# Optimization experiments

Hardware: AMD Instinct MI355X
Metric: run time of the kernel (lower is better)

## Reference

```python
import jax, jax.numpy as jnp
import numpy as np


def _ln(x, g, b, eps=1e-5):
    mu = jnp.mean(x, axis=-1, keepdims=True)
    var = jnp.mean((x - mu) ** 2, axis=-1, keepdims=True)
    return (x - mu) / jnp.sqrt(var + eps) * g + b


def _cell(x, h, c, Wih, Whh, bih, bhh):
    # torch LSTM gate order: i, f, g, o
    gates = x @ Wih.T + h @ Whh.T + bih + bhh
    i, f, g, o = jnp.split(gates, 4, axis=-1)
    c_new = jax.nn.sigmoid(f) * c + jax.nn.sigmoid(i) * jnp.tanh(g)
    h_new = jax.nn.sigmoid(o) * jnp.tanh(c_new)
    return h_new, c_new


def _forward(physical, target_seq, enc_W1, enc_b1, enc_ln1_g, enc_ln1_b, enc_W2, enc_b2,
             enc_ln2_g, enc_ln2_b, Wih0, Whh0, bih0, bhh0, Wih1, Whh1, bih1, bhh1,
             ln_g, ln_b, proj_W, proj_b, head_W1, head_b1, head_W2, head_b2, init_input):
    B, T = target_seq.shape
    Hd = proj_b.shape[0]
    # physical encoder -> initial hidden (dropout in eval mode)
    e = jax.nn.relu(_ln(physical @ enc_W1.T + enc_b1, enc_ln1_g, enc_ln1_b))
    h0 = jnp.tanh(_ln(e @ enc_W2.T + enc_b2, enc_ln2_g, enc_ln2_b))  # (B,H)
    h_init = jnp.broadcast_to(h0, (2, 2, B, Hd))  # (layer, direction, B, H)
    c_init = jnp.zeros((2, 2, B, Hd), dtype=h0.dtype)
    # teacher forcing ratio = 1.0 -> inputs are known ahead of time
    x0 = jnp.broadcast_to(init_input, (B, 1))
    xs = jnp.concatenate([x0[None], jnp.swapaxes(target_seq, 0, 1)[:-1, :, None]], axis=0)  # (T,B,1)

    def step(carry, inp):
        h, c, prev = carry
        x, t = inp
        h0f, c0f = _cell(x, h[0, 0], c[0, 0], Wih0[0], Whh0[0], bih0[0], bhh0[0])
        h0b, c0b = _cell(x, h[0, 1], c[0, 1], Wih0[1], Whh0[1], bih0[1], bhh0[1])
        o0 = jnp.concatenate([h0f, h0b], axis=-1)  # (B,2H)
        h1f, c1f = _cell(o0, h[1, 0], c[1, 0], Wih1[0], Whh1[0], bih1[0], bhh1[0])
        h1b, c1b = _cell(o0, h[1, 1], c[1, 1], Wih1[1], Whh1[1], bih1[1], bhh1[1])
        out = _ln(jnp.concatenate([h1f, h1b], axis=-1), ln_g, ln_b)  # (B,2H)
        proj = out @ proj_W.T + proj_b  # (B,H)
        pred = jax.nn.relu(proj @ head_W1.T + head_b1) @ head_W2.T + head_b2  # (B,1)
        pred = jnp.where(t > 0, 0.8 * pred + 0.2 * prev, pred)
        h_new = jnp.stack([jnp.stack([h0f, h0b]), jnp.stack([h1f, h1b])])
        c_new = jnp.stack([jnp.stack([c0f, c0b]), jnp.stack([c1f, c1b])])
        return (h_new, c_new, pred), pred[:, 0]

    _, preds = jax.lax.scan(step, (h_init, c_init, jnp.zeros((B, 1), h0.dtype)),
                            (xs, jnp.arange(T)))
    return jnp.swapaxes(preds, 0, 1)  # (B,T)


def setup_inputs():
    B, P, Hd, T = 512, 16, 128, 128
    ks = iter(jax.random.split(jax.random.key(0), 40))
    rn = lambda shape, s=0.05: jax.random.normal(next(ks), shape, dtype=jnp.float32) * s
    return {
        "physical": jax.random.normal(next(ks), (B, P), dtype=jnp.float32),
        "target_seq": jax.random.normal(next(ks), (B, T), dtype=jnp.float32),
        "enc_W1": rn((2 * Hd, P)), "enc_b1": jnp.zeros((2 * Hd,), jnp.float32),
        "enc_ln1_g": jnp.ones((2 * Hd,), jnp.float32), "enc_ln1_b": jnp.zeros((2 * Hd,), jnp.float32),
        "enc_W2": rn((Hd, 2 * Hd)), "enc_b2": jnp.zeros((Hd,), jnp.float32),
        "enc_ln2_g": jnp.ones((Hd,), jnp.float32), "enc_ln2_b": jnp.zeros((Hd,), jnp.float32),
        "Wih0": rn((2, 4 * Hd, 1)), "Whh0": rn((2, 4 * Hd, Hd)),
        "bih0": jnp.zeros((2, 4 * Hd), jnp.float32), "bhh0": jnp.zeros((2, 4 * Hd), jnp.float32),
        "Wih1": rn((2, 4 * Hd, 2 * Hd)), "Whh1": rn((2, 4 * Hd, Hd)),
        "bih1": jnp.zeros((2, 4 * Hd), jnp.float32), "bhh1": jnp.zeros((2, 4 * Hd), jnp.float32),
        "ln_g": jnp.ones((2 * Hd,), jnp.float32), "ln_b": jnp.zeros((2 * Hd,), jnp.float32),
        "proj_W": rn((Hd, 2 * Hd)), "proj_b": jnp.zeros((Hd,), jnp.float32),
        "head_W1": rn((Hd, Hd)), "head_b1": jnp.zeros((Hd,), jnp.float32),
        "head_W2": rn((1, Hd)), "head_b2": jnp.zeros((1,), jnp.float32),
        "init_input": rn((1,), 0.02),
    }


def reference(physical, target_seq, enc_W1, enc_b1, enc_ln1_g, enc_ln1_b, enc_W2, enc_b2,
              enc_ln2_g, enc_ln2_b, Wih0, Whh0, bih0, bhh0, Wih1, Whh1, bih1, bhh1,
              ln_g, ln_b, proj_W, proj_b, head_W1, head_b1, head_W2, head_b2, init_input):
    return _forward(physical, target_seq, enc_W1, enc_b1, enc_ln1_g, enc_ln1_b, enc_W2, enc_b2,
                    enc_ln2_g, enc_ln2_b, Wih0, Whh0, bih0, bhh0, Wih1, Whh1, bih1, bhh1,
                    ln_g, ln_b, proj_W, proj_b, head_W1, head_b1, head_W2, head_b2, init_input)
```

## Files before the change

### kernel.cpp

```cpp
#include <hip/hip_runtime.h>
#include <hip/hip_bf16.h>

#define BB 512
#define TT 128

typedef unsigned short u16;
typedef short v8s __attribute__((ext_vector_type(8)));
typedef float f32x4 __attribute__((ext_vector_type(4)));

__device__ __forceinline__ u16 f2bf(float x){
  union { float f; unsigned int u; } v; v.f = x;
  unsigned int r = (v.u + 0x7fffu + ((v.u >> 16) & 1u)) >> 16;
  return (u16)r;
}
__device__ __forceinline__ float bf2f(u16 u){
  union { unsigned int i; float f; } v; v.i = ((unsigned int)u) << 16; return v.f;
}
__device__ __forceinline__ uint2 pack4(f32x4 a){
  uint2 r;
  r.x = (unsigned)f2bf(a[0]) | ((unsigned)f2bf(a[1]) << 16);
  r.y = (unsigned)f2bf(a[2]) | ((unsigned)f2bf(a[3]) << 16);
  return r;
}
__device__ __forceinline__ float rcp_f(float x){ return __builtin_amdgcn_rcpf(x); }
__device__ __forceinline__ float sigm(float x){
  return rcp_f(1.f + __expf(-x));
}
__device__ __forceinline__ float tanh_f(float x){
  float e = __expf(-2.f * fabsf(x));
  float r = (1.f - e) * rcp_f(1.f + e);
  return copysignf(r, x);
}
__device__ __forceinline__ void bar_lds(){
  __builtin_amdgcn_sched_barrier(0);
  asm volatile("s_waitcnt lgkmcnt(0)" ::: "memory");
  __builtin_amdgcn_s_barrier();
  __builtin_amdgcn_sched_barrier(0);
}

__global__ __launch_bounds__(256) void k_prep(
    const float* tseq, const float* init_in,
    const float* Wih0, const float* Whh0, const float* bih0, const float* bhh0,
    const float* Wih1, const float* Whh1, const float* bih1, const float* bhh1,
    const float* projW, const float* hW1,
    float* xs, u16* W0p, u16* W1ip, u16* W1hp, u16* projWp, u16* hW1p,
    float* bias0, float* bias1, float* wv0)
{
  int tid = blockIdx.x * blockDim.x + threadIdx.x;
  int stride = gridDim.x * blockDim.x;
  for (int i = tid; i < TT*BB; i += stride){
    int t = i / BB, b = i % BB;
    xs[i] = (t == 0) ? init_in[0] : tseq[b*TT + (t-1)];
  }
  for (int i = tid; i < 2*512*128; i += stride){
    int d = i / (512*128), r = i % (512*128);
    int j = r / 128, k = r % 128;
    int dst = ((((d*32 + (j>>4))*4 + (k>>5))*64) + ((j&15) + 16*((k&31)>>3)))*8 + (k&7);
    W0p[dst]  = f2bf(Whh0[i]);
    W1hp[dst] = f2bf(Whh1[i]);
  }
  for (int i = tid; i < 2*512*256; i += stride){
    int d = i / (512*256), r = i % (512*256);
    int j = r / 256, k = r % 256;
    int dst = ((((d*32 + (j>>4))*8 + (k>>5))*64) + ((j&15) + 16*((k&31)>>3)))*8 + (k&7);
    W1ip[dst] = f2bf(Wih1[i]);
  }
  for (int i = tid; i < 128*256; i += stride){
    int j = i / 256, k = i % 256;
    int dst = ((((j>>4)*8 + (k>>5))*64) + ((j&15) + 16*((k&31)>>3)))*8 + (k&7);
    projWp[dst] = f2bf(projW[i]);
  }
  for (int i = tid; i < 128*128; i += stride){
    int j = i / 128, k = i % 128;
    int dst = ((((j>>4)*4 + (k>>5))*64) + ((j&15) + 16*((k&31)>>3)))*8 + (k&7);
    hW1p[dst] = f2bf(hW1[i]);
  }
  for (int i = tid; i < 2*512; i += stride){
    bias0[i] = bih0[i] + bhh0[i];
    bias1[i] = bih1[i] + bhh1[i];
    wv0[i]   = Wih0[i];
  }
}

__global__ __launch_bounds__(256) void k_enc(
    const float* phys, const float* W1, const float* b1, const float* g1, const float* be1,
    const float* W2, const float* b2, const float* g2, const float* be2, float* h0enc)
{
  __shared__ float eL[8][256];
  int tid = threadIdx.x;
  int rr = tid >> 5, sub = tid & 31;
  int r = blockIdx.x * 8 + rr;
  float x[16];
#pragma unroll
  for (int k = 0; k < 16; ++k) x[k] = phys[r*16 + k];
  float y[8];
#pragma unroll
  for (int jj = 0; jj < 8; ++jj){
    int j = sub*8 + jj;
    float s = b1[j];
#pragma unroll
    for (int k = 0; k < 16; ++k) s += x[k] * W1[j*16 + k];
    y[jj] = s;
  }
  float sum = 0.f, sq = 0.f;
#pragma unroll
  for (int jj = 0; jj < 8; ++jj){ sum += y[jj]; sq += y[jj]*y[jj]; }
#pragma unroll
  for (int m = 16; m >= 1; m >>= 1){ sum += __shfl_xor(sum, m, 32); sq += __shfl_xor(sq, m, 32); }
  float mu = sum / 256.f;
  float rs = rsqrtf(sq / 256.f - mu*mu + 1e-5f);
#pragma unroll
  for (int jj = 0; jj < 8; ++jj){
    int j = sub*8 + jj;
    eL[rr][j] = fmaxf((y[jj] - mu) * rs * g1[j] + be1[j], 0.f);
  }
  __syncthreads();
  float y2[4];
#pragma unroll
  for (int jj = 0; jj < 4; ++jj){
    int j2 = sub*4 + jj;
    float s = b2[j2];
    const float* wrow = W2 + j2*256;
    for (int k = 0; k < 256; k += 4)
      s += eL[rr][k]*wrow[k] + eL[rr][k+1]*wrow[k+1] + eL[rr][k+2]*wrow[k+2] + eL[rr][k+3]*wrow[k+3];
    y2[jj] = s;
  }
  sum = 0.f; sq = 0.f;
#pragma unroll
  for (int jj = 0; jj < 4; ++jj){ sum += y2[jj]; sq += y2[jj]*y2[jj]; }
#pragma unroll
  for (int m = 16; m >= 1; m >>= 1){ sum += __shfl_xor(sum, m, 32); sq += __shfl_xor(sq, m, 32); }
  mu = sum / 128.f;
  rs = rsqrtf(sq / 128.f - mu*mu + 1e-5f);
#pragma unroll
  for (int jj = 0; jj < 4; ++jj){
    int j2 = sub*4 + jj;
    h0enc[r*128 + j2] = tanh_f((y2[jj]-mu)*rs*g2[j2] + be2[j2]);
  }
}

__global__ __launch_bounds__(512, 2) void k_l0(
    const u16* W0p, const float* bias0, const float* wv0, const float* xs,
    const float* h0enc, u16* o0pack)
{
  __shared__ __align__(16) u16 Xb[2][4][512];
  __shared__ __align__(16) float xl[TT*16];
  int bx = blockIdx.x;
  int tile = bx & 31, d = bx >> 5;
  int tid = threadIdx.x, w = tid >> 6, l = tid & 63;
  int r0 = tile * 16, lrow = l & 15, lk = l >> 4;

  for (int i = tid; i < TT*16; i += 512){
    int t = i >> 4, r = i & 15;
    xl[i] = xs[t*BB + r0 + r];
  }
  if (tid < 256){
    int kf = tid >> 6, ll = tid & 63;
    const float* src = h0enc + (r0 + (ll & 15))*128 + kf*32 + 8*(ll >> 4);
    u16* dstp = &Xb[0][kf][ll*8];
#pragma unroll
    for (int i = 0; i < 8; ++i) dstp[i] = f2bf(src[i]);
  }

  const u16* Wb = W0p + (size_t)d*32*4*512;
  v8s wa[4][4];
#pragma unroll
  for (int q = 0; q < 4; ++q)
#pragma unroll
    for (int kf = 0; kf < 4; ++kf)
      wa[q][kf] = *(const v8s*)(Wb + (size_t)(((w + 8*q)*4 + kf)*64 + l)*8);

  float bias[4][4], wv[4][4];
#pragma unroll
  for (int q = 0; q < 4; ++q){
    int tq = w + 8*q;
#pragma unroll
    for (int jj = 0; jj < 4; ++jj){
      int j = tq*16 + 4*lk + jj;
      bias[q][jj] = bias0[d*512 + j];
      wv[q][jj]   = wv0[d*512 + j];
    }
  }
  float c[4] = {0.f,0.f,0.f,0.f};
  int jout = w*16 + 4*lk;
  int kfx = jout >> 5;
  int sl  = lrow + 16*((jout & 31) >> 3);
  int eb  = jout & 7;
  int kfo = 4*d + kfx;
  __syncthreads();

  for (int t = 0; t < TT; ++t){
    int cur = t & 1, nxt = cur ^ 1;
    v8s bfr[4];
#pragma unroll
    for (int kf = 0; kf < 4; ++kf) bfr[kf] = *(const v8s*)&Xb[cur][kf][l*8];
    float xv = xl[t*16 + lrow];
    f32x4 acc[4];
#pragma unroll
    for (int q = 0; q < 4; ++q)
#pragma unroll
      for (int jj = 0; jj < 4; ++jj)
        acc[q][jj] = fmaf(xv, wv[q][jj], bias[q][jj]);
#pragma unroll
    for (int kf = 0; kf < 4; ++kf)
#pragma unroll
      for (int q = 0; q < 4; ++q)
        acc[q] = __builtin_amdgcn_mfma_f32_16x16x32_bf16(wa[q][kf], bfr[kf], acc[q], 0, 0, 0);
    float hn[4];
#pragma unroll
    for (int jj = 0; jj < 4; ++jj){
      float si = sigm(acc[0][jj]);
      float sf = sigm(acc[1][jj]);
      float tg = tanh_f(acc[2][jj]);
      float so = sigm(acc[3][jj]);
      float cn = fmaf(sf, c[jj], si*tg);
      c[jj] = cn;
      hn[jj] = so * tanh_f(cn);
    }
    uint2 hp;
    hp.x = (unsigned)f2bf(hn[0]) | ((unsigned)f2bf(hn[1]) << 16);
    hp.y = (unsigned)f2bf(hn[2]) | ((unsigned)f2bf(hn[3]) << 16);
    *(uint2*)&Xb[nxt][kfx][sl*8 + eb] = hp;
    size_t off = ((((size_t)t*32 + tile)*8 + kfo)*64 + sl)*8 + eb;
    *(uint2*)&o0pack[off] = hp;
    bar_lds();
  }
}

__global__ __launch_bounds__(256) void k_zgemm(
    const u16* W1ip, const u16* o0pack, u16* z1p)
{
  int bx = blockIdx.x;
  int nc = bx & 3, bg = (bx >> 2) & 7, t = bx >> 5;
  int w = threadIdx.x >> 6, l = threadIdx.x & 63;
  int btile = bg*4 + w;
  v8s bfrag[8];
#pragma unroll
  for (int kf = 0; kf < 8; ++kf)
    bfrag[kf] = *(const v8s*)&o0pack[((((size_t)t*32 + btile)*8 + kf)*64 + l)*8];
  f32x4 acc[16];
#pragma unroll
  for (int nt = 0; nt < 16; ++nt) acc[nt] = (f32x4){0.f,0.f,0.f,0.f};
#pragma unroll
  for (int kf = 0; kf < 8; ++kf){
#pragma unroll
    for (int nt = 0; nt < 16; ++nt){
      int ntg = nc*16 + nt;
      int dir = ntg >> 5, tl = ntg & 31;
      v8s a = *(const v8s*)&W1ip[((((size_t)dir*32 + tl)*8 + kf)*64 + l)*8];
      acc[nt] = __builtin_amdgcn_mfma_f32_16x16x32_bf16(a, bfrag[kf], acc[nt], 0, 0, 0);
    }
  }
#pragma unroll
  for (int nt = 0; nt < 16; ++nt){
    int ntg = nc*16 + nt;
    uint2 zp = pack4(acc[nt]);
    *(uint2*)&z1p[((((size_t)t*32 + btile)*64 + ntg)*64 + l)*4] = zp;
  }
}

__global__ __launch_bounds__(512, 2) void k_l1(
    const u16* W1hp, const float* bias1, const u16* z1p,
    const float* h0enc, u16* h1b)
{
  __shared__ __align__(16) u16 Xh[2][4][512];
  int bx = blockIdx.x;
  int tile = bx & 31, d = bx >> 5;
  int tid = threadIdx.x, w = tid >> 6, l = tid & 63;
  int r0 = tile * 16, lrow = l & 15, lk = l >> 4;

  if (tid < 256){
    int kf = tid >> 6, ll = tid & 63;
    const float* src = h0enc + (r0 + (ll & 15))*128 + kf*32 + 8*(ll >> 4);
    u16* dstp = &Xh[0][kf][ll*8];
#pragma unroll
    for (int i = 0; i < 8; ++i) dstp[i] = f2bf(src[i]);
  }

  const u16* Wh = W1hp + (size_t)d*32*4*512;
  v8s wh[4][4];
#pragma unroll
  for (int q = 0; q < 4; ++q)
#pragma unroll
    for (int kf = 0; kf < 4; ++kf)
      wh[q][kf] = *(const v8s*)(Wh + (size_t)(((w + 8*q)*4 + kf)*64 + l)*8);

  float bias[4][4];
#pragma unroll
  for (int q = 0; q < 4; ++q)
#pragma unroll
    for (int jj = 0; jj < 4; ++jj)
      bias[q][jj] = bias1[d*512 + (w + 8*q)*16 + 4*lk + jj];

  float c[4] = {0.f,0.f,0.f,0.f};
  int jout = w*16 + 4*lk;
  int kfx = jout >> 5;
  int sl  = lrow + 16*((jout & 31) >> 3);
  int eb  = jout & 7;

  uint2 zr[4];
#pragma unroll
  for (int q = 0; q < 4; ++q)
    zr[q] = *(const uint2*)&z1p[(((size_t)tile*64 + d*32 + w + 8*q)*64 + l)*4];
  __syncthreads();

  for (int t = 0; t < TT; ++t){
    int cur = t & 1, nxt = cur ^ 1;
    int tn = (t + 1 < TT) ? t + 1 : t;
    uint2 zn[4];
#pragma unroll
    for (int q = 0; q < 4; ++q)
      zn[q] = *(const uint2*)&z1p[((((size_t)tn*32 + tile)*64 + d*32 + w + 8*q)*64 + l)*4];
    v8s bh[4];
#pragma unroll
    for (int kf = 0; kf < 4; ++kf) bh[kf] = *(const v8s*)&Xh[cur][kf][l*8];
    f32x4 acc[4];
#pragma unroll
    for (int q = 0; q < 4; ++q){
      acc[q][0] = bias[q][0] + bf2f((u16)(zr[q].x & 0xffffu));
      acc[q][1] = bias[q][1] + bf2f((u16)(zr[q].x >> 16));
      acc[q][2] = bias[q][2] + bf2f((u16)(zr[q].y & 0xffffu));
      acc[q][3] = bias[q][3] + bf2f((u16)(zr[q].y >> 16));
    }
#pragma unroll
    for (int kf = 0; kf < 4; ++kf)
#pragma unroll
      for (int q = 0; q < 4; ++q)
        acc[q] = __builtin_amdgcn_mfma_f32_16x16x32_bf16(wh[q][kf], bh[kf], acc[q], 0, 0, 0);
    float hn[4];
#pragma unroll
    for (int jj = 0; jj < 4; ++jj){
      float si = sigm(acc[0][jj]);
      float sf = sigm(acc[1][jj]);
      float tg = tanh_f(acc[2][jj]);
      float so = sigm(acc[3][jj]);
      float cn = fmaf(sf, c[jj], si*tg);
      c[jj] = cn;
      hn[jj] = so * tanh_f(cn);
    }
    uint2 hp;
    hp.x = (unsigned)f2bf(hn[0]) | ((unsigned)f2bf(hn[1]) << 16);
    hp.y = (unsigned)f2bf(hn[2]) | ((unsigned)f2bf(hn[3]) << 16);
    *(uint2*)&Xh[nxt][kfx][sl*8 + eb] = hp;
    int hidx = ((t*BB + r0 + lrow) << 8) + (d << 7) + jout;
    *(uint2*)&h1b[hidx] = hp;
#pragma unroll
    for (int q = 0; q < 4; ++q) zr[q] = zn[q];
    bar_lds();
  }
}

__global__ __launch_bounds__(256) void k_head(
    const u16* h1b, const float* lng, const float* lnb,
    const u16* projWp, const float* projb,
    const u16* hW1p, const float* hb1, const float* hW2, const float* hb2,
    float* qout)
{
  __shared__ __align__(16) u16 xls[4][16*256];
  __shared__ __align__(16) u16 pls[4][16*128];
  int w = threadIdx.x >> 6, l = threadIdx.x & 63;
  size_t g0 = (size_t)blockIdx.x*64 + w*16;
  int row = l >> 2, qc = l & 3;

  const u16* srcb = h1b + (g0 + row)*256;
  f32x4 v[16];
#pragma unroll
  for (int m = 0; m < 16; ++m){
    uint2 p = *(const uint2*)&srcb[m*16 + qc*4];
    v[m][0] = bf2f((u16)(p.x & 0xffffu));
    v[m][1] = bf2f((u16)(p.x >> 16));
    v[m][2] = bf2f((u16)(p.y & 0xffffu));
    v[m][3] = bf2f((u16)(p.y >> 16));
  }
  float sum = 0.f, sq = 0.f;
#pragma unroll
  for (int m = 0; m < 16; ++m){
#pragma unroll
    for (int i = 0; i < 4; ++i){ sum += v[m][i]; sq += v[m][i]*v[m][i]; }
  }
  sum += __shfl_xor(sum, 1); sq += __shfl_xor(sq, 1);
  sum += __shfl_xor(sum, 2); sq += __shfl_xor(sq, 2);
  float mu = sum / 256.f;
  float rs = rsqrtf(sq / 256.f - mu*mu + 1e-5f);
  u16* xw = xls[w];
  int rsw = (row & 7) << 3;
#pragma unroll
  for (int m = 0; m < 16; ++m){
    int cb = m*16 + qc*4;
    f32x4 gq = *(const f32x4*)&lng[cb];
    f32x4 bq = *(const f32x4*)&lnb[cb];
    f32x4 xn;
#pragma unroll
    for (int i = 0; i < 4; ++i) xn[i] = (v[m][i]-mu)*rs*gq[i] + bq[i];
    *(uint2*)&xw[(row*256 + cb) ^ rsw] = pack4(xn);
  }

  int lk = l >> 4, r = l & 15;
  int rsw2 = (r & 7) << 3;
  f32x4 acc[8];
#pragma unroll
  for (int nt = 0; nt < 8; ++nt) acc[nt] = *(const f32x4*)&projb[nt*16 + lk*4];
#pragma unroll
  for (int kf = 0; kf < 8; ++kf){
    v8s b = *(const v8s*)&xw[(r*256 + kf*32 + lk*8) ^ rsw2];
#pragma unroll
    for (int nt = 0; nt < 8; ++nt){
      v8s a = *(const v8s*)&projWp[(((size_t)nt*8 + kf)*64 + l)*8];
      acc[nt] = __builtin_amdgcn_mfma_f32_16x16x32_bf16(a, b, acc[nt], 0, 0, 0);
    }
  }
  u16* pw = pls[w];
#pragma unroll
  for (int nt = 0; nt < 8; ++nt)
    *(uint2*)&pw[(r*128 + nt*16 + lk*4) ^ rsw2] = pack4(acc[nt]);

  f32x4 acc2[8];
#pragma unroll
  for (int nt = 0; nt < 8; ++nt) acc2[nt] = *(const f32x4*)&hb1[nt*16 + lk*4];
#pragma unroll
  for (int kf = 0; kf < 4; ++kf){
    v8s b = *(const v8s*)&pw[(r*128 + kf*32 + lk*8) ^ rsw2];
#pragma unroll
    for (int nt = 0; nt < 8; ++nt){
      v8s a = *(const v8s*)&hW1p[(((size_t)nt*4 + kf)*64 + l)*8];
      acc2[nt] = __builtin_amdgcn_mfma_f32_16x16x32_bf16(a, b, acc2[nt], 0, 0, 0);
    }
  }
  float part = 0.f;
#pragma unroll
  for (int nt = 0; nt < 8; ++nt){
    f32x4 w2 = *(const f32x4*)&hW2[nt*16 + lk*4];
#pragma unroll
    for (int jj = 0; jj < 4; ++jj) part += fmaxf(acc2[nt][jj], 0.f) * w2[jj];
  }
  part += __shfl_xor(part, 16);
  part += __shfl_xor(part, 32);
  if (l < 16) qout[g0 + l] = part + hb2[0];
}

__global__ __launch_bounds__(512) void k_blend(const float* qout, float* out)
{
  int b = threadIdx.x;
  float pred = 0.f;
  for (int t0 = 0; t0 < TT; t0 += 16){
    float v[16];
#pragma unroll
    for (int i = 0; i < 16; ++i) v[i] = qout[(t0+i)*BB + b];
#pragma unroll
    for (int i = 0; i < 16; ++i){
      pred = (t0 + i == 0) ? v[i] : 0.8f*v[i] + 0.2f*pred;
      out[b*TT + t0 + i] = pred;
    }
  }
}

extern "C" void kernel_launch(void* const* d_in, const int* in_sizes, int n_in,
                              void* d_out, int out_size, void* d_ws, size_t ws_size,
                              hipStream_t stream) {
  const float* physical   = (const float*)d_in[0];
  const float* target_seq = (const float*)d_in[1];
  const float* enc_W1     = (const float*)d_in[2];
  const float* enc_b1     = (const float*)d_in[3];
  const float* enc_ln1_g  = (const float*)d_in[4];
  const float* enc_ln1_b  = (const float*)d_in[5];
  const float* enc_W2     = (const float*)d_in[6];
  const float* enc_b2     = (const float*)d_in[7];
  const float* enc_ln2_g  = (const float*)d_in[8];
  const float* enc_ln2_b  = (const float*)d_in[9];
  const float* Wih0       = (const float*)d_in[10];
  const float* Whh0       = (const float*)d_in[11];
  const float* bih0       = (const float*)d_in[12];
  const float* bhh0       = (const float*)d_in[13];
  const float* Wih1       = (const float*)d_in[14];
  const float* Whh1       = (const float*)d_in[15];
  const float* bih1       = (const float*)d_in[16];
  const float* bhh1       = (const float*)d_in[17];
  const float* ln_g       = (const float*)d_in[18];
  const float* ln_b       = (const float*)d_in[19];
  const float* proj_W     = (const float*)d_in[20];
  const float* proj_b     = (const float*)d_in[21];
  const float* head_W1    = (const float*)d_in[22];
  const float* head_b1    = (const float*)d_in[23];
  const float* head_W2    = (const float*)d_in[24];
  const float* head_b2    = (const float*)d_in[25];
  const float* init_input = (const float*)d_in[26];

  size_t off = 0;
  char* base = (char*)d_ws;
  auto carve = [&](size_t bytes) -> void* {
    void* p = base + off;
    off += (bytes + 255) & ~(size_t)255;
    return p;
  };
  u16*   o0pack  = (u16*)  carve((size_t)TT*32*8*64*8*2);
  u16*   h1b     = (u16*)  carve((size_t)TT*BB*256*2);
  u16*   z1p     = (u16*)  carve((size_t)TT*32*64*64*4*2);
  float* qout    = (float*)carve((size_t)TT*BB*4);
  float* h0enc   = (float*)carve((size_t)BB*128*4);
  float* xs      = (float*)carve((size_t)TT*BB*4);
  u16*   W0p     = (u16*)  carve((size_t)2*512*128*2);
  u16*   W1ip    = (u16*)  carve((size_t)2*512*256*2);
  u16*   W1hp    = (u16*)  carve((size_t)2*512*128*2);
  u16*   projWp  = (u16*)  carve((size_t)128*256*2);
  u16*   hW1p    = (u16*)  carve((size_t)128*128*2);
  float* bias0   = (float*)carve(4096);
  float* bias1   = (float*)carve(4096);
  float* wv0     = (float*)carve(4096);

  k_prep<<<256, 256, 0, stream>>>(target_seq, init_input, Wih0, Whh0, bih0, bhh0,
                                  Wih1, Whh1, bih1, bhh1, proj_W, head_W1,
                                  xs, W0p, W1ip, W1hp, projWp, hW1p,
                                  bias0, bias1, wv0);
  k_enc<<<64, 256, 0, stream>>>(physical, enc_W1, enc_b1, enc_ln1_g, enc_ln1_b,
                                enc_W2, enc_b2, enc_ln2_g, enc_ln2_b, h0enc);
  k_l0<<<64, 512, 0, stream>>>(W0p, bias0, wv0, xs, h0enc, o0pack);
  k_zgemm<<<4096, 256, 0, stream>>>(W1ip, o0pack, z1p);
  k_l1<<<64, 512, 0, stream>>>(W1hp, bias1, z1p, h0enc, h1b);
  k_head<<<1024, 256, 0, stream>>>(h1b, ln_g, ln_b, projWp, proj_b,
                                   hW1p, head_b1, head_W2, head_b2, qout);
  k_blend<<<1, 512, 0, stream>>>(qout, (float*)d_out);
}
```

Before: 428.3 us.

## Fold log2e into LSTM weights, use exp2 activations, prefetch z, move bias

Pre-scales the LSTM gate weights and biases by log2(e) (2*log2(e) for the g gate) so the sigmoid and tanh calls become bare exp2 plus reciprocal, with tanh written as 2*sigmoid-1. It also uses the hardware packed bf16 convert, cheaper bf16 unpacking, and folds bias1 into the z-GEMM accumulator init. The layer-1 recurrence now prefetches z two steps ahead instead of one, and both recurrent loops drop the occupancy hint and unroll by 2. Together these aim to shorten the serial per-step critical path of the recurrence. In exchange there is a slight accuracy change from scaling before bf16 rounding, and possible register-pressure shifts from the unroll and launch-bound change.

```diff
diff --git a/kernel.cpp b/kernel.cpp
--- a/kernel.cpp
+++ b/kernel.cpp
@@ -7,6 +7,9 @@
 typedef unsigned short u16;
 typedef short v8s __attribute__((ext_vector_type(8)));
 typedef float f32x4 __attribute__((ext_vector_type(4)));
+
+#define L2E  1.4426950408889634f
+#define L2E2 2.8853900817779268f
 
 __device__ __forceinline__ u16 f2bf(float x){
   union { float f; unsigned int u; } v; v.f = x;
@@ -16,16 +19,33 @@
 __device__ __forceinline__ float bf2f(u16 u){
   union { unsigned int i; float f; } v; v.i = ((unsigned int)u) << 16; return v.f;
 }
+__device__ __forceinline__ float lo_bits(unsigned u){
+  union { unsigned int i; float f; } v; v.i = u << 16; return v.f;
+}
+__device__ __forceinline__ float hi_bits(unsigned u){
+  union { unsigned int i; float f; } v; v.i = u & 0xffff0000u; return v.f;
+}
 __device__ __forceinline__ uint2 pack4(f32x4 a){
   uint2 r;
-  r.x = (unsigned)f2bf(a[0]) | ((unsigned)f2bf(a[1]) << 16);
-  r.y = (unsigned)f2bf(a[2]) | ((unsigned)f2bf(a[3]) << 16);
+  asm("v_cvt_pk_bf16_f32 %0, %1, %2" : "=v"(r.x) : "v"(a[0]), "v"(a[1]));
+  asm("v_cvt_pk_bf16_f32 %0, %1, %2" : "=v"(r.y) : "v"(a[2]), "v"(a[3]));
   return r;
 }
 __device__ __forceinline__ float rcp_f(float x){ return __builtin_amdgcn_rcpf(x); }
-__device__ __forceinline__ float sigm(float x){
-  return rcp_f(1.f + __expf(-x));
-}
+#if defined(__has_builtin)
+#if __has_builtin(__builtin_amdgcn_exp2f)
+#define EXP2(x) __builtin_amdgcn_exp2f(x)
+#endif
+#endif
+#ifndef EXP2
+__device__ __forceinline__ float __exp2_asm(float x){
+  float r; asm("v_exp_f32 %0, %1" : "=v"(r) : "v"(x)); return r;
+}
+#define EXP2(x) __exp2_asm(x)
+#endif
+__device__ __forceinline__ float sigm2(float y){ return rcp_f(1.f + EXP2(-y)); }
+__device__ __forceinline__ float tanh2(float y){ return fmaf(2.f, sigm2(y), -1.f); }
+
 __device__ __forceinline__ float tanh_f(float x){
   float e = __expf(-2.f * fabsf(x));
   float r = (1.f - e) * rcp_f(1.f + e);
@@ -55,15 +75,17 @@
   for (int i = tid; i < 2*512*128; i += stride){
     int d = i / (512*128), r = i % (512*128);
     int j = r / 128, k = r % 128;
+    float sc = ((j >> 7) == 2) ? L2E2 : L2E;
     int dst = ((((d*32 + (j>>4))*4 + (k>>5))*64) + ((j&15) + 16*((k&31)>>3)))*8 + (k&7);
-    W0p[dst]  = f2bf(Whh0[i]);
-    W1hp[dst] = f2bf(Whh1[i]);
+    W0p[dst]  = f2bf(Whh0[i] * sc);
+    W1hp[dst] = f2bf(Whh1[i] * sc);
   }
   for (int i = tid; i < 2*512*256; i += stride){
     int d = i / (512*256), r = i % (512*256);
     int j = r / 256, k = r % 256;
+    float sc = ((j >> 7) == 2) ? L2E2 : L2E;
     int dst = ((((d*32 + (j>>4))*8 + (k>>5))*64) + ((j&15) + 16*((k&31)>>3)))*8 + (k&7);
-    W1ip[dst] = f2bf(Wih1[i]);
+    W1ip[dst] = f2bf(Wih1[i] * sc);
   }
   for (int i = tid; i < 128*256; i += stride){
     int j = i / 256, k = i % 256;
@@ -76,9 +98,10 @@
     hW1p[dst] = f2bf(hW1[i]);
   }
   for (int i = tid; i < 2*512; i += stride){
-    bias0[i] = bih0[i] + bhh0[i];
-    bias1[i] = bih1[i] + bhh1[i];
-    wv0[i]   = Wih0[i];
+    float sc = (((i & 511) >> 7) == 2) ? L2E2 : L2E;
+    bias0[i] = (bih0[i] + bhh0[i]) * sc;
+    bias1[i] = (bih1[i] + bhh1[i]) * sc;
+    wv0[i]   = Wih0[i] * sc;
   }
 }
 
@@ -139,7 +162,7 @@
   }
 }
 
-__global__ __launch_bounds__(512, 2) void k_l0(
+__global__ __launch_bounds__(512) void k_l0(
     const u16* W0p, const float* bias0, const float* wv0, const float* xs,
     const float* h0enc, u16* o0pack)
 {
@@ -189,6 +212,7 @@
   int kfo = 4*d + kfx;
   __syncthreads();
 
+#pragma unroll 2
   for (int t = 0; t < TT; ++t){
     int cur = t & 1, nxt = cur ^ 1;
     v8s bfr[4];
@@ -206,20 +230,19 @@
 #pragma unroll
       for (int q = 0; q < 4; ++q)
         acc[q] = __builtin_amdgcn_mfma_f32_16x16x32_bf16(wa[q][kf], bfr[kf], acc[q], 0, 0, 0);
-    float hn[4];
+    f32x4 hv;
 #pragma unroll
     for (int jj = 0; jj < 4; ++jj){
-      float si = sigm(acc[0][jj]);
-      float sf = sigm(acc[1][jj]);
-      float tg = tanh_f(acc[2][jj]);
-      float so = sigm(acc[3][jj]);
+      float si = sigm2(acc[0][jj]);
+      float sf = sigm2(acc[1][jj]);
+      float tg = tanh2(acc[2][jj]);
+      float so = sigm2(acc[3][jj]);
       float cn = fmaf(sf, c[jj], si*tg);
       c[jj] = cn;
-      hn[jj] = so * tanh_f(cn);
-    }
-    uint2 hp;
-    hp.x = (unsigned)f2bf(hn[0]) | ((unsigned)f2bf(hn[1]) << 16);
-    hp.y = (unsigned)f2bf(hn[2]) | ((unsigned)f2bf(hn[3]) << 16);
+      float s2 = sigm2(L2E2 * cn);
+      hv[jj] = so * fmaf(2.f, s2, -1.f);
+    }
+    uint2 hp = pack4(hv);
     *(uint2*)&Xb[nxt][kfx][sl*8 + eb] = hp;
     size_t off = ((((size_t)t*32 + tile)*8 + kfo)*64 + sl)*8 + eb;
     *(uint2*)&o0pack[off] = hp;
@@ -228,19 +251,23 @@
 }
 
 __global__ __launch_bounds__(256) void k_zgemm(
-    const u16* W1ip, const u16* o0pack, u16* z1p)
+    const u16* W1ip, const float* bias1p, const u16* o0pack, u16* z1p)
 {
   int bx = blockIdx.x;
   int nc = bx & 3, bg = (bx >> 2) & 7, t = bx >> 5;
   int w = threadIdx.x >> 6, l = threadIdx.x & 63;
   int btile = bg*4 + w;
+  int lk4 = (l >> 4) * 4;
   v8s bfrag[8];
 #pragma unroll
   for (int kf = 0; kf < 8; ++kf)
     bfrag[kf] = *(const v8s*)&o0pack[((((size_t)t*32 + btile)*8 + kf)*64 + l)*8];
   f32x4 acc[16];
 #pragma unroll
-  for (int nt = 0; nt < 16; ++nt) acc[nt] = (f32x4){0.f,0.f,0.f,0.f};
+  for (int nt = 0; nt < 16; ++nt){
+    int ntg = nc*16 + nt;
+    acc[nt] = *(const f32x4*)&bias1p[(ntg >> 5)*512 + (ntg & 31)*16 + lk4];
+  }
 #pragma unroll
   for (int kf = 0; kf < 8; ++kf){
 #pragma unroll
@@ -259,9 +286,8 @@
   }
 }
 
-__global__ __launch_bounds__(512, 2) void k_l1(
-    const u16* W1hp, const float* bias1, const u16* z1p,
-    const float* h0enc, u16* h1b)
+__global__ __launch_bounds__(512) void k_l1(
+    const u16* W1hp, const u16* z1p, const float* h0enc, u16* h1b)
 {
   __shared__ __align__(16) u16 Xh[2][4][512];
   int bx = blockIdx.x;
@@ -285,67 +311,63 @@
     for (int kf = 0; kf < 4; ++kf)
       wh[q][kf] = *(const v8s*)(Wh + (size_t)(((w + 8*q)*4 + kf)*64 + l)*8);
 
-  float bias[4][4];
-#pragma unroll
-  for (int q = 0; q < 4; ++q)
-#pragma unroll
-    for (int jj = 0; jj < 4; ++jj)
-      bias[q][jj] = bias1[d*512 + (w + 8*q)*16 + 4*lk + jj];
-
   float c[4] = {0.f,0.f,0.f,0.f};
   int jout = w*16 + 4*lk;
   int kfx = jout >> 5;
   int sl  = lrow + 16*((jout & 31) >> 3);
   int eb  = jout & 7;
-
-  uint2 zr[4];
+  int zcol = d*32 + w;
+
+  uint2 zr[4], zn[4];
 #pragma unroll
   for (int q = 0; q < 4; ++q)
-    zr[q] = *(const uint2*)&z1p[(((size_t)tile*64 + d*32 + w + 8*q)*64 + l)*4];
+    zr[q] = *(const uint2*)&z1p[(((size_t)tile*64 + zcol + 8*q)*64 + l)*4];
+#pragma unroll
+  for (int q = 0; q < 4; ++q)
+    zn[q] = *(const uint2*)&z1p[((((size_t)1*32 + tile)*64 + zcol + 8*q)*64 + l)*4];
   __syncthreads();
 
+#pragma unroll 2
   for (int t = 0; t < TT; ++t){
     int cur = t & 1, nxt = cur ^ 1;
-    int tn = (t + 1 < TT) ? t + 1 : t;
-    uint2 zn[4];
-#pragma unroll
-    for (int q = 0; q < 4; ++q)
-      zn[q] = *(const uint2*)&z1p[((((size_t)tn*32 + tile)*64 + d*32 + w + 8*q)*64 + l)*4];
     v8s bh[4];
 #pragma unroll
     for (int kf = 0; kf < 4; ++kf) bh[kf] = *(const v8s*)&Xh[cur][kf][l*8];
     f32x4 acc[4];
 #pragma unroll
     for (int q = 0; q < 4; ++q){
-      acc[q][0] = bias[q][0] + bf2f((u16)(zr[q].x & 0xffffu));
-      acc[q][1] = bias[q][1] + bf2f((u16)(zr[q].x >> 16));
-      acc[q][2] = bias[q][2] + bf2f((u16)(zr[q].y & 0xffffu));
-      acc[q][3] = bias[q][3] + bf2f((u16)(zr[q].y >> 16));
+      acc[q][0] = lo_bits(zr[q].x);
+      acc[q][1] = hi_bits(zr[q].x);
+      acc[q][2] = lo_bits(zr[q].y);
+      acc[q][3] = hi_bits(zr[q].y);
     }
 #pragma unroll
     for (int kf = 0; kf < 4; ++kf)
 #pragma unroll
       for (int q = 0; q < 4; ++q)
         acc[q] = __builtin_amdgcn_mfma_f32_16x16x32_bf16(wh[q][kf], bh[kf], acc[q], 0, 0, 0);
-    float hn[4];
+    f32x4 hv;
 #pragma unroll
     for (int jj = 0; jj < 4; ++jj){
-      float si = sigm(acc[0][jj]);
-      float sf = sigm(acc[1][jj]);
-      float tg = tanh_f(acc[2][jj]);
-      float so = sigm(acc[3][jj]);
+      float si = sigm2(acc[0][jj]);
+      float sf = sigm2(acc[1][jj]);
+      float tg = tanh2(acc[2][jj]);
+      float so = sigm2(acc[3][jj]);
       float cn = fmaf(sf, c[jj], si*tg);
       c[jj] = cn;
-      hn[jj] = so * tanh_f(cn);
-    }
-    uint2 hp;
-    hp.x = (unsigned)f2bf(hn[0]) | ((unsigned)f2bf(hn[1]) << 16);
-    hp.y = (unsigned)f2bf(hn[2]) | ((unsigned)f2bf(hn[3]) << 16);
+      float s2 = sigm2(L2E2 * cn);
+      hv[jj] = so * fmaf(2.f, s2, -1.f);
+    }
+    uint2 hp = pack4(hv);
     *(uint2*)&Xh[nxt][kfx][sl*8 + eb] = hp;
     int hidx = ((t*BB + r0 + lrow) << 8) + (d << 7) + jout;
     *(uint2*)&h1b[hidx] = hp;
 #pragma unroll
     for (int q = 0; q < 4; ++q) zr[q] = zn[q];
+    int tp = (t + 2 < TT) ? t + 2 : TT - 1;
+#pragma unroll
+    for (int q = 0; q < 4; ++q)
+      zn[q] = *(const uint2*)&z1p[((((size_t)tp*32 + tile)*64 + zcol + 8*q)*64 + l)*4];
     bar_lds();
   }
 }
@@ -367,10 +389,10 @@
 #pragma unroll
   for (int m = 0; m < 16; ++m){
     uint2 p = *(const uint2*)&srcb[m*16 + qc*4];
-    v[m][0] = bf2f((u16)(p.x & 0xffffu));
-    v[m][1] = bf2f((u16)(p.x >> 16));
-    v[m][2] = bf2f((u16)(p.y & 0xffffu));
-    v[m][3] = bf2f((u16)(p.y >> 16));
+    v[m][0] = lo_bits(p.x);
+    v[m][1] = hi_bits(p.x);
+    v[m][2] = lo_bits(p.y);
+    v[m][3] = hi_bits(p.y);
   }
   float sum = 0.f, sq = 0.f;
 #pragma unroll
@@ -514,8 +536,8 @@
   k_enc<<<64, 256, 0, stream>>>(physical, enc_W1, enc_b1, enc_ln1_g, enc_ln1_b,
                                 enc_W2, enc_b2, enc_ln2_g, enc_ln2_b, h0enc);
   k_l0<<<64, 512, 0, stream>>>(W0p, bias0, wv0, xs, h0enc, o0pack);
-  k_zgemm<<<4096, 256, 0, stream>>>(W1ip, o0pack, z1p);
-  k_l1<<<64, 512, 0, stream>>>(W1hp, bias1, z1p, h0enc, h1b);
+  k_zgemm<<<4096, 256, 0, stream>>>(W1ip, bias1, o0pack, z1p);
+  k_l1<<<64, 512, 0, stream>>>(W1hp, z1p, h0enc, h1b);
   k_head<<<1024, 256, 0, stream>>>(h1b, ln_g, ln_b, projWp, proj_b,
                                    hW1p, head_b1, head_W2, head_b2, qout);
   k_blend<<<1, 512, 0, stream>>>(qout, (float*)d_out);
```

Result: faster. 376.7 us (-12.0%).
